# Optimization experiments

Hardware: AMD Instinct MI355X
Metric: run time of the kernel (lower is better)

The kernel has to match this reference:

```python
import jax, jax.numpy as jnp
import numpy as np

B, E, H, T = 32768, 64, 128, 12  # batch, embedding_dim, decoder_h_dim, pred_len


def setup_inputs() -> dict:
    key = jax.random.key(0)
    ks = jax.random.split(key, 13)
    f = lambda k, shape: jax.random.normal(k, shape, dtype=jnp.float32) * 0.05
    return {
        "last_pos": f(ks[0], (B, 2)),
        "last_pos_rel": f(ks[1], (B, 2)),
        "h0": f(ks[2], (1, B, H)),
        "c0": f(ks[3], (1, B, H)),
        "pred_ped_speed": jax.random.uniform(ks[4], (T, B, 1), dtype=jnp.float32),
        # spatial_embedding: Linear(3, E)
        "W_se": f(ks[5], (E, 3)),
        "b_se": f(ks[6], (E,)),
        # single-layer LSTM(E -> H), torch gate order [i, f, g, o]
        "W_ih": f(ks[7], (4 * H, E)),
        "W_hh": f(ks[8], (4 * H, H)),
        "b_ih": f(ks[9], (4 * H,)),
        "b_hh": f(ks[10], (4 * H,)),
        # hidden2pos: Linear(H, 2)
        "W_hp": f(ks[11], (2, H)),
        "b_hp": f(ks[12], (2,)),
    }


def reference(last_pos, last_pos_rel, h0, c0, pred_ped_speed,
              W_se, b_se, W_ih, W_hh, b_ih, b_hh, W_hp, b_hp):
    # train_or_test == 0 path: speed comes straight from pred_ped_speed
    Tlen = pred_ped_speed.shape[0]
    b_lstm = b_ih + b_hh
    # initial decoder input: embed concat([last_pos_rel, speed_0])  -> [B, E]
    x0 = jnp.concatenate([last_pos_rel, pred_ped_speed[0]], axis=1) @ W_se.T + b_se

    def step(carry, t):
        h, c, x, lp = carry  # h,c: [B,H]; x: [B,E]; lp: [B,2]
        gates = x @ W_ih.T + h @ W_hh.T + b_lstm           # [B, 4H]
        i, f_, g, o = jnp.split(gates, 4, axis=1)
        c = jax.nn.sigmoid(f_) * c + jax.nn.sigmoid(i) * jnp.tanh(g)
        h = jax.nn.sigmoid(o) * jnp.tanh(c)
        rel = h @ W_hp.T + b_hp                            # [B, 2]
        lp = rel + lp                                      # curr_pos -> last_pos
        # speed for next step; at final step torch keeps the previous speed
        spd = pred_ped_speed[jnp.minimum(t + 1, Tlen - 1)]
        x = jnp.concatenate([rel, spd], axis=1) @ W_se.T + b_se
        return (h, c, x, lp), rel

    (h, c, _, _), rels = jax.lax.scan(
        step, (h0[0], c0[0], x0, last_pos), jnp.arange(Tlen))
    # pred_traj_fake_rel: [T, B, 2]; final hidden state: [1, B, H]
    return rels, h[None]
```

## Files before the change

### kernel.cpp

```cpp
#include <hip/hip_runtime.h>

#define T_LEN 12
#define B_N   32768
#define H_N   128
#define E_N   64
#define K_N   192
#define LDK   200
#define BM    64

typedef __attribute__((ext_vector_type(8))) __bf16 bf16x8;
typedef __attribute__((ext_vector_type(8))) short  short8v;
typedef __attribute__((ext_vector_type(4))) float  f32x4;

__device__ __forceinline__ unsigned short f2bf(float f) {
  unsigned int u = __builtin_bit_cast(unsigned int, f);
  u += 0x7fffu + ((u >> 16) & 1u);
  return (unsigned short)(u >> 16);
}
__device__ __forceinline__ float bf2f(unsigned short h) {
  unsigned int u = ((unsigned int)h) << 16;
  return __builtin_bit_cast(float, u);
}
__device__ __forceinline__ float sigm(float x) {
  return __builtin_amdgcn_rcpf(1.f + __builtin_amdgcn_exp2f(-1.4426950408889634f * x));
}
__device__ __forceinline__ float tanh_(float x) {
  return 1.f - 2.f * __builtin_amdgcn_rcpf(__builtin_amdgcn_exp2f(2.8853900817779268f * x) + 1.f);
}

__global__ void prep_kernel(const float* __restrict__ Wih, const float* __restrict__ Whh,
                            const float* __restrict__ bih, const float* __restrict__ bhh,
                            unsigned short* __restrict__ Wc, float* __restrict__ bl) {
  int i = blockIdx.x * 256 + threadIdx.x;
  if (i < 4 * H_N) bl[i] = bih[i] + bhh[i];
  if (i < 4 * H_N * K_N) {
    int n = i / K_N, k = i - n * K_N;
    float v = (k < E_N) ? Wih[n * E_N + k] : Whh[n * H_N + (k - E_N)];
    Wc[i] = f2bf(v);
  }
}

__launch_bounds__(512, 2)
__global__ void decoder_kernel(const float* __restrict__ last_pos_rel,
                               const float* __restrict__ h0,
                               const float* __restrict__ c0,
                               const float* __restrict__ pps,
                               const float* __restrict__ W_se,
                               const float* __restrict__ b_se,
                               const float* __restrict__ W_hp,
                               const float* __restrict__ b_hp,
                               const unsigned short* __restrict__ Wc,
                               const float* __restrict__ bl,
                               float* __restrict__ out_rel,
                               float* __restrict__ out_h) {
  __shared__ unsigned short xh[BM * LDK];
  __shared__ float relbuf[BM * 2];
  __shared__ float whp[2 * H_N];

  const int tid  = threadIdx.x;
  const int w    = tid >> 6;
  const int l    = tid & 63;
  const int l15  = l & 15;
  const int lg   = l >> 4;
  const int brow = blockIdx.x * BM;
  const int nh   = w * 16 + l15;

  short8v bw[4][6];
#pragma unroll
  for (int g = 0; g < 4; ++g)
#pragma unroll
    for (int ks = 0; ks < 6; ++ks)
      bw[g][ks] = *(const short8v*)(Wc + (g * H_N + nh) * K_N + ks * 32 + lg * 8);

  float bgate[4];
#pragma unroll
  for (int g = 0; g < 4; ++g) bgate[g] = bl[g * H_N + nh];

  f32x4 cst[4];
#pragma unroll
  for (int mt = 0; mt < 4; ++mt)
#pragma unroll
    for (int r = 0; r < 4; ++r)
      cst[mt][r] = c0[(brow + mt * 16 + lg * 4 + r) * H_N + nh];

  if (tid < 2 * H_N) whp[tid] = W_hp[tid];
  for (int i = tid; i < BM * H_N; i += 512) {
    int row = i >> 7, n = i & (H_N - 1);
    xh[row * LDK + E_N + n] = f2bf(h0[(brow + row) * H_N + n]);
  }
  const int  xe   = tid & 63;
  const float wse0 = W_se[xe * 3 + 0], wse1 = W_se[xe * 3 + 1], wse2 = W_se[xe * 3 + 2];
  const float bse  = b_se[xe];
  const float bhp0 = b_hp[0], bhp1 = b_hp[1];

#pragma unroll
  for (int rr = 0; rr < 8; ++rr) {
    int row = (tid >> 6) * 8 + rr;
    float r0 = last_pos_rel[(brow + row) * 2 + 0];
    float r1 = last_pos_rel[(brow + row) * 2 + 1];
    float sp = pps[0 * B_N + brow + row];
    xh[row * LDK + xe] = f2bf(r0 * wse0 + r1 * wse1 + sp * wse2 + bse);
  }

#pragma unroll 1
  for (int t = 0; t < T_LEN; ++t) {
    __syncthreads();

    f32x4 acc[4][4];
#pragma unroll
    for (int g = 0; g < 4; ++g)
#pragma unroll
      for (int mt = 0; mt < 4; ++mt)
        acc[g][mt] = (f32x4){bgate[g], bgate[g], bgate[g], bgate[g]};

#pragma unroll
    for (int ks = 0; ks < 6; ++ks) {
      bf16x8 a[4];
#pragma unroll
      for (int mt = 0; mt < 4; ++mt)
        a[mt] = __builtin_bit_cast(bf16x8,
                 *(const short8v*)(xh + (mt * 16 + l15) * LDK + ks * 32 + lg * 8));
#pragma unroll
      for (int g = 0; g < 4; ++g)
#pragma unroll
        for (int mt = 0; mt < 4; ++mt)
          acc[g][mt] = __builtin_amdgcn_mfma_f32_16x16x32_bf16(
              a[mt], __builtin_bit_cast(bf16x8, bw[g][ks]), acc[g][mt], 0, 0, 0);
    }

    __syncthreads();

#pragma unroll
    for (int mt = 0; mt < 4; ++mt) {
#pragma unroll
      for (int r = 0; r < 4; ++r) {
        float gi = acc[0][mt][r], gf = acc[1][mt][r];
        float gg = acc[2][mt][r], go = acc[3][mt][r];
        float cn = sigm(gf) * cst[mt][r] + sigm(gi) * tanh_(gg);
        cst[mt][r] = cn;
        float h = sigm(go) * tanh_(cn);
        int row = mt * 16 + lg * 4 + r;
        xh[row * LDK + E_N + nh] = f2bf(h);
        if (t == T_LEN - 1) out_h[(brow + row) * H_N + nh] = h;
      }
    }

    __syncthreads();

    {
      int dot = tid >> 2, part = tid & 3;
      int row = dot >> 1, j = dot & 1;
      float s = 0.f;
      int n0 = part * 32;
#pragma unroll
      for (int n = 0; n < 32; ++n)
        s += bf2f(xh[row * LDK + E_N + n0 + n]) * whp[j * H_N + n0 + n];
      s += __shfl_xor(s, 1);
      s += __shfl_xor(s, 2);
      if (part == 0) relbuf[dot] = s + (j ? bhp1 : bhp0);
    }

    __syncthreads();

    if (tid < 2 * BM) out_rel[(size_t)t * B_N * 2 + brow * 2 + tid] = relbuf[tid];
    if (t < T_LEN - 1) {
#pragma unroll
      for (int rr = 0; rr < 8; ++rr) {
        int row = (tid >> 6) * 8 + rr;
        float r0 = relbuf[row * 2 + 0], r1 = relbuf[row * 2 + 1];
        float sp = pps[(t + 1) * B_N + brow + row];
        xh[row * LDK + xe] = f2bf(r0 * wse0 + r1 * wse1 + sp * wse2 + bse);
      }
    }
  }
}

extern "C" void kernel_launch(void* const* d_in, const int* in_sizes, int n_in,
                              void* d_out, int out_size, void* d_ws, size_t ws_size,
                              hipStream_t stream) {
  const float* last_pos_rel = (const float*)d_in[1];
  const float* h0   = (const float*)d_in[2];
  const float* c0   = (const float*)d_in[3];
  const float* pps  = (const float*)d_in[4];
  const float* W_se = (const float*)d_in[5];
  const float* b_se = (const float*)d_in[6];
  const float* W_ih = (const float*)d_in[7];
  const float* W_hh = (const float*)d_in[8];
  const float* b_ih = (const float*)d_in[9];
  const float* b_hh = (const float*)d_in[10];
  const float* W_hp = (const float*)d_in[11];
  const float* b_hp = (const float*)d_in[12];

  unsigned short* Wc = (unsigned short*)d_ws;
  float* bl = (float*)((char*)d_ws + (size_t)(4 * H_N) * K_N * sizeof(unsigned short));

  float* out_rel = (float*)d_out;
  float* out_h   = out_rel + (size_t)T_LEN * B_N * 2;

  hipLaunchKernelGGL(prep_kernel, dim3((4 * H_N * K_N + 255) / 256), dim3(256), 0, stream,
                     W_ih, W_hh, b_ih, b_hh, Wc, bl);
  hipLaunchKernelGGL(decoder_kernel, dim3(B_N / BM), dim3(512), 0, stream,
                     last_pos_rel, h0, c0, pps, W_se, b_se, W_hp, b_hp, Wc, bl,
                     out_rel, out_h);
}
```

Baseline: 263.5 us.

## Fold input embedding and hidden2pos into recurrent weights, halve block rows

Folds the spatial embedding and hidden2pos projections algebraically into a single 512x128 recurrent matrix, so each step multiplies only h (K=128 instead of 192), plus a per-row speed term and a first-step correction. Half of the fused weights now live in swizzled LDS and half in registers. The rel output is computed with an extra small MFMA one step later. The block tile drops to 32 rows with launch bounds raised to 4 blocks per CU, and two per-step barriers plus the scalar dot-product pass are removed. The folded weights are rounded to bf16 after combining, which shifts numerical error slightly.

```diff
diff --git a/kernel.cpp b/kernel.cpp
--- a/kernel.cpp
+++ b/kernel.cpp
@@ -4,9 +4,7 @@
 #define B_N   32768
 #define H_N   128
 #define E_N   64
-#define K_N   192
-#define LDK   200
-#define BM    64
+#define BM    32
 
 typedef __attribute__((ext_vector_type(8))) __bf16 bf16x8;
 typedef __attribute__((ext_vector_type(8))) short  short8v;
@@ -17,10 +15,6 @@
   u += 0x7fffu + ((u >> 16) & 1u);
   return (unsigned short)(u >> 16);
 }
-__device__ __forceinline__ float bf2f(unsigned short h) {
-  unsigned int u = ((unsigned int)h) << 16;
-  return __builtin_bit_cast(float, u);
-}
 __device__ __forceinline__ float sigm(float x) {
   return __builtin_amdgcn_rcpf(1.f + __builtin_amdgcn_exp2f(-1.4426950408889634f * x));
 }
@@ -30,32 +24,54 @@
 
 __global__ void prep_kernel(const float* __restrict__ Wih, const float* __restrict__ Whh,
                             const float* __restrict__ bih, const float* __restrict__ bhh,
-                            unsigned short* __restrict__ Wc, float* __restrict__ bl) {
+                            const float* __restrict__ Wse, const float* __restrict__ bse,
+                            const float* __restrict__ Whp, const float* __restrict__ bhp,
+                            unsigned short* __restrict__ Wf, float* __restrict__ u,
+                            float* __restrict__ w0, float* __restrict__ G) {
   int i = blockIdx.x * 256 + threadIdx.x;
-  if (i < 4 * H_N) bl[i] = bih[i] + bhh[i];
-  if (i < 4 * H_N * K_N) {
-    int n = i / K_N, k = i - n * K_N;
-    float v = (k < E_N) ? Wih[n * E_N + k] : Whh[n * H_N + (k - E_N)];
-    Wc[i] = f2bf(v);
-  }
-}
-
-__launch_bounds__(512, 2)
-__global__ void decoder_kernel(const float* __restrict__ last_pos_rel,
+  if (i < 512 * 128) {
+    int n = i >> 7, k = i & 127;
+    float s = Whh[n * 128 + k];
+    float wh0 = Whp[k], wh1 = Whp[128 + k];
+    for (int e = 0; e < 64; ++e)
+      s += Wih[n * 64 + e] * (Wse[e * 3 + 0] * wh0 + Wse[e * 3 + 1] * wh1);
+    Wf[i] = f2bf(s);
+  } else if (i < 512 * 128 + 2048) {
+    int j = i - 512 * 128;
+    int n = j >> 2, which = j & 3;
+    float s = 0.f;
+    if (which < 2) {
+      for (int e = 0; e < 64; ++e) s += Wih[n * 64 + e] * Wse[e * 3 + which];
+      G[n * 2 + which] = s;
+    } else if (which == 2) {
+      for (int e = 0; e < 64; ++e) s += Wih[n * 64 + e] * Wse[e * 3 + 2];
+      u[n] = s;
+    } else {
+      for (int e = 0; e < 64; ++e)
+        s += Wih[n * 64 + e] * (bse[e] + Wse[e * 3 + 0] * bhp[0] + Wse[e * 3 + 1] * bhp[1]);
+      w0[n] = bih[n] + bhh[n] + s;
+    }
+  }
+}
+
+__launch_bounds__(512, 4)
+__global__ void decoder_kernel(const float* __restrict__ lpr,
                                const float* __restrict__ h0,
                                const float* __restrict__ c0,
                                const float* __restrict__ pps,
-                               const float* __restrict__ W_se,
-                               const float* __restrict__ b_se,
-                               const float* __restrict__ W_hp,
-                               const float* __restrict__ b_hp,
-                               const unsigned short* __restrict__ Wc,
-                               const float* __restrict__ bl,
+                               const float* __restrict__ Whp,
+                               const float* __restrict__ bhp,
+                               const unsigned short* __restrict__ Wf,
+                               const float* __restrict__ u,
+                               const float* __restrict__ w0,
+                               const float* __restrict__ G,
                                float* __restrict__ out_rel,
                                float* __restrict__ out_h) {
-  __shared__ unsigned short xh[BM * LDK];
-  __shared__ float relbuf[BM * 2];
-  __shared__ float whp[2 * H_N];
+  __shared__ unsigned short WfL[256 * 128];
+  __shared__ unsigned short hS[BM * 128];
+  __shared__ unsigned short whpB[4 * 64 * 8];
+  __shared__ float spdbuf[BM];
+  __shared__ float dbuf[BM * 2];
 
   const int tid  = threadIdx.x;
   const int w    = tid >> 6;
@@ -64,113 +80,147 @@
   const int lg   = l >> 4;
   const int brow = blockIdx.x * BM;
   const int nh   = w * 16 + l15;
-
-  short8v bw[4][6];
-#pragma unroll
-  for (int g = 0; g < 4; ++g)
-#pragma unroll
-    for (int ks = 0; ks < 6; ++ks)
-      bw[g][ks] = *(const short8v*)(Wc + (g * H_N + nh) * K_N + ks * 32 + lg * 8);
-
-  float bgate[4];
-#pragma unroll
-  for (int g = 0; g < 4; ++g) bgate[g] = bl[g * H_N + nh];
-
-  f32x4 cst[4];
-#pragma unroll
-  for (int mt = 0; mt < 4; ++mt)
+  const int swz  = (l15 & 7) << 4;
+  char* hB  = (char*)hS;
+  char* wB  = (char*)WfL;
+  char* pB  = (char*)whpB;
+
+  for (int i = tid; i < 256 * 16; i += 512) {
+    int row = i >> 4, k16 = i & 15;
+    short8v v = *(const short8v*)(Wf + (256 + row) * 128 + k16 * 8);
+    int byte = (row * 256 + k16 * 16) ^ ((row & 7) << 4);
+    *(short8v*)(wB + byte) = v;
+  }
+  short8v bw[2][4];
+#pragma unroll
+  for (int g = 0; g < 2; ++g)
+#pragma unroll
+    for (int ks = 0; ks < 4; ++ks)
+      bw[g][ks] = *(const short8v*)(Wf + (g * 128 + nh) * 128 + ks * 32 + lg * 8);
+
+  float ur[4], w0r[4];
+#pragma unroll
+  for (int g = 0; g < 4; ++g) { ur[g] = u[g * 128 + nh]; w0r[g] = w0[g * 128 + nh]; }
+
+  f32x4 cst[2];
+#pragma unroll
+  for (int mt = 0; mt < 2; ++mt)
 #pragma unroll
     for (int r = 0; r < 4; ++r)
       cst[mt][r] = c0[(brow + mt * 16 + lg * 4 + r) * H_N + nh];
 
-  if (tid < 2 * H_N) whp[tid] = W_hp[tid];
-  for (int i = tid; i < BM * H_N; i += 512) {
-    int row = i >> 7, n = i & (H_N - 1);
-    xh[row * LDK + E_N + n] = f2bf(h0[(brow + row) * H_N + n]);
-  }
-  const int  xe   = tid & 63;
-  const float wse0 = W_se[xe * 3 + 0], wse1 = W_se[xe * 3 + 1], wse2 = W_se[xe * 3 + 2];
-  const float bse  = b_se[xe];
-  const float bhp0 = b_hp[0], bhp1 = b_hp[1];
-
-#pragma unroll
-  for (int rr = 0; rr < 8; ++rr) {
-    int row = (tid >> 6) * 8 + rr;
-    float r0 = last_pos_rel[(brow + row) * 2 + 0];
-    float r1 = last_pos_rel[(brow + row) * 2 + 1];
-    float sp = pps[0 * B_N + brow + row];
-    xh[row * LDK + xe] = f2bf(r0 * wse0 + r1 * wse1 + sp * wse2 + bse);
-  }
+  {
+    int row = tid >> 4, k0 = (tid & 15) * 8;
+    const float* src = h0 + (brow + row) * H_N + k0;
+    unsigned short tmp[8];
+#pragma unroll
+    for (int j = 0; j < 8; ++j) tmp[j] = f2bf(src[j]);
+    int byte = (row * 256 + k0 * 2) ^ ((row & 7) << 4);
+    *(short8v*)(hB + byte) = *(short8v*)tmp;
+  }
+  if (tid < 256) {
+    int ks = tid >> 6, ll = tid & 63, c = ll & 15, kg = ll >> 4;
+    unsigned short tmp[8];
+#pragma unroll
+    for (int j = 0; j < 8; ++j)
+      tmp[j] = (c < 2) ? f2bf(Whp[c * 128 + ks * 32 + kg * 8 + j]) : (unsigned short)0;
+    *(short8v*)(pB + (ks * 64 + ll) * 16) = *(short8v*)tmp;
+  }
+  {
+    int dot = tid >> 3, part = tid & 7;
+    int row = dot >> 1, j = dot & 1;
+    float s = 0.f;
+    const float* hrow = h0 + (brow + row) * H_N + part * 16;
+    const float* wrow = Whp + j * 128 + part * 16;
+#pragma unroll
+    for (int k = 0; k < 16; ++k) s += hrow[k] * wrow[k];
+    s += __shfl_xor(s, 1); s += __shfl_xor(s, 2); s += __shfl_xor(s, 4);
+    if (part == 0) dbuf[dot] = lpr[(brow + row) * 2 + j] - bhp[j] - s;
+  }
+  const float bhpr = (l15 < 2) ? bhp[l15] : 0.f;
 
 #pragma unroll 1
   for (int t = 0; t < T_LEN; ++t) {
     __syncthreads();
 
-    f32x4 acc[4][4];
+    if (tid < BM) spdbuf[tid] = pps[t * B_N + brow + tid];
+
+    f32x4 acc[4][2];
 #pragma unroll
     for (int g = 0; g < 4; ++g)
 #pragma unroll
-      for (int mt = 0; mt < 4; ++mt)
-        acc[g][mt] = (f32x4){bgate[g], bgate[g], bgate[g], bgate[g]};
-
-#pragma unroll
-    for (int ks = 0; ks < 6; ++ks) {
-      bf16x8 a[4];
-#pragma unroll
-      for (int mt = 0; mt < 4; ++mt)
-        a[mt] = __builtin_bit_cast(bf16x8,
-                 *(const short8v*)(xh + (mt * 16 + l15) * LDK + ks * 32 + lg * 8));
-#pragma unroll
-      for (int g = 0; g < 4; ++g)
-#pragma unroll
-        for (int mt = 0; mt < 4; ++mt)
-          acc[g][mt] = __builtin_amdgcn_mfma_f32_16x16x32_bf16(
-              a[mt], __builtin_bit_cast(bf16x8, bw[g][ks]), acc[g][mt], 0, 0, 0);
+      for (int mt = 0; mt < 2; ++mt) acc[g][mt] = (f32x4){0.f, 0.f, 0.f, 0.f};
+    f32x4 relC = (f32x4){0.f, 0.f, 0.f, 0.f};
+
+#pragma unroll
+    for (int ks = 0; ks < 4; ++ks) {
+      int kb = ks * 64 + lg * 16;
+      bf16x8 a0 = __builtin_bit_cast(bf16x8, *(short8v*)(hB + ((l15 * 256 + kb) ^ swz)));
+      bf16x8 a1 = __builtin_bit_cast(bf16x8, *(short8v*)(hB + (((16 + l15) * 256 + kb) ^ swz)));
+      bf16x8 b2 = __builtin_bit_cast(bf16x8, *(short8v*)(wB + ((nh * 256 + kb) ^ swz)));
+      bf16x8 b3 = __builtin_bit_cast(bf16x8, *(short8v*)(wB + 32768 + ((nh * 256 + kb) ^ swz)));
+      acc[0][0] = __builtin_amdgcn_mfma_f32_16x16x32_bf16(a0, __builtin_bit_cast(bf16x8, bw[0][ks]), acc[0][0], 0, 0, 0);
+      acc[0][1] = __builtin_amdgcn_mfma_f32_16x16x32_bf16(a1, __builtin_bit_cast(bf16x8, bw[0][ks]), acc[0][1], 0, 0, 0);
+      acc[1][0] = __builtin_amdgcn_mfma_f32_16x16x32_bf16(a0, __builtin_bit_cast(bf16x8, bw[1][ks]), acc[1][0], 0, 0, 0);
+      acc[1][1] = __builtin_amdgcn_mfma_f32_16x16x32_bf16(a1, __builtin_bit_cast(bf16x8, bw[1][ks]), acc[1][1], 0, 0, 0);
+      acc[2][0] = __builtin_amdgcn_mfma_f32_16x16x32_bf16(a0, b2, acc[2][0], 0, 0, 0);
+      acc[2][1] = __builtin_amdgcn_mfma_f32_16x16x32_bf16(a1, b2, acc[2][1], 0, 0, 0);
+      acc[3][0] = __builtin_amdgcn_mfma_f32_16x16x32_bf16(a0, b3, acc[3][0], 0, 0, 0);
+      acc[3][1] = __builtin_amdgcn_mfma_f32_16x16x32_bf16(a1, b3, acc[3][1], 0, 0, 0);
+      if (w < 2 && t > 0) {
+        bf16x8 wb = __builtin_bit_cast(bf16x8, *(short8v*)(pB + ks * 1024 + l * 16));
+        relC = __builtin_amdgcn_mfma_f32_16x16x32_bf16(w == 0 ? a0 : a1, wb, relC, 0, 0, 0);
+      }
+    }
+    if (w < 2 && t > 0 && l15 < 2) {
+#pragma unroll
+      for (int r = 0; r < 4; ++r)
+        out_rel[(size_t)(t - 1) * B_N * 2 + (brow + w * 16 + lg * 4 + r) * 2 + l15] = relC[r] + bhpr;
     }
 
     __syncthreads();
 
 #pragma unroll
-    for (int mt = 0; mt < 4; ++mt) {
+    for (int mt = 0; mt < 2; ++mt) {
 #pragma unroll
       for (int r = 0; r < 4; ++r) {
-        float gi = acc[0][mt][r], gf = acc[1][mt][r];
-        float gg = acc[2][mt][r], go = acc[3][mt][r];
+        int row = mt * 16 + lg * 4 + r;
+        float spd = spdbuf[row];
+        float gi = acc[0][mt][r] + w0r[0] + spd * ur[0];
+        float gf = acc[1][mt][r] + w0r[1] + spd * ur[1];
+        float gg = acc[2][mt][r] + w0r[2] + spd * ur[2];
+        float go = acc[3][mt][r] + w0r[3] + spd * ur[3];
+        if (t == 0) {
+          float d0 = dbuf[row * 2 + 0], d1 = dbuf[row * 2 + 1];
+          gi += d0 * G[(0 * 128 + nh) * 2 + 0] + d1 * G[(0 * 128 + nh) * 2 + 1];
+          gf += d0 * G[(1 * 128 + nh) * 2 + 0] + d1 * G[(1 * 128 + nh) * 2 + 1];
+          gg += d0 * G[(2 * 128 + nh) * 2 + 0] + d1 * G[(2 * 128 + nh) * 2 + 1];
+          go += d0 * G[(3 * 128 + nh) * 2 + 0] + d1 * G[(3 * 128 + nh) * 2 + 1];
+        }
         float cn = sigm(gf) * cst[mt][r] + sigm(gi) * tanh_(gg);
         cst[mt][r] = cn;
         float h = sigm(go) * tanh_(cn);
-        int row = mt * 16 + lg * 4 + r;
-        xh[row * LDK + E_N + nh] = f2bf(h);
+        hS[((row * 256 + nh * 2) ^ ((row & 7) << 4)) >> 1] = f2bf(h);
         if (t == T_LEN - 1) out_h[(brow + row) * H_N + nh] = h;
       }
     }
-
-    __syncthreads();
-
-    {
-      int dot = tid >> 2, part = tid & 3;
-      int row = dot >> 1, j = dot & 1;
-      float s = 0.f;
-      int n0 = part * 32;
-#pragma unroll
-      for (int n = 0; n < 32; ++n)
-        s += bf2f(xh[row * LDK + E_N + n0 + n]) * whp[j * H_N + n0 + n];
-      s += __shfl_xor(s, 1);
-      s += __shfl_xor(s, 2);
-      if (part == 0) relbuf[dot] = s + (j ? bhp1 : bhp0);
-    }
-
-    __syncthreads();
-
-    if (tid < 2 * BM) out_rel[(size_t)t * B_N * 2 + brow * 2 + tid] = relbuf[tid];
-    if (t < T_LEN - 1) {
-#pragma unroll
-      for (int rr = 0; rr < 8; ++rr) {
-        int row = (tid >> 6) * 8 + rr;
-        float r0 = relbuf[row * 2 + 0], r1 = relbuf[row * 2 + 1];
-        float sp = pps[(t + 1) * B_N + brow + row];
-        xh[row * LDK + xe] = f2bf(r0 * wse0 + r1 * wse1 + sp * wse2 + bse);
-      }
+  }
+
+  __syncthreads();
+  if (w < 2) {
+    f32x4 relC = (f32x4){0.f, 0.f, 0.f, 0.f};
+#pragma unroll
+    for (int ks = 0; ks < 4; ++ks) {
+      int kb = ks * 64 + lg * 16;
+      bf16x8 a = __builtin_bit_cast(bf16x8,
+          *(short8v*)(hB + (((w * 16 + l15) * 256 + kb) ^ swz)));
+      bf16x8 wb = __builtin_bit_cast(bf16x8, *(short8v*)(pB + ks * 1024 + l * 16));
+      relC = __builtin_amdgcn_mfma_f32_16x16x32_bf16(a, wb, relC, 0, 0, 0);
+    }
+    if (l15 < 2) {
+#pragma unroll
+      for (int r = 0; r < 4; ++r)
+        out_rel[(size_t)(T_LEN - 1) * B_N * 2 + (brow + w * 16 + lg * 4 + r) * 2 + l15] = relC[r] + bhpr;
     }
   }
 }
@@ -178,7 +228,7 @@
 extern "C" void kernel_launch(void* const* d_in, const int* in_sizes, int n_in,
                               void* d_out, int out_size, void* d_ws, size_t ws_size,
                               hipStream_t stream) {
-  const float* last_pos_rel = (const float*)d_in[1];
+  const float* lpr  = (const float*)d_in[1];
   const float* h0   = (const float*)d_in[2];
   const float* c0   = (const float*)d_in[3];
   const float* pps  = (const float*)d_in[4];
@@ -191,15 +241,16 @@
   const float* W_hp = (const float*)d_in[11];
   const float* b_hp = (const float*)d_in[12];
 
-  unsigned short* Wc = (unsigned short*)d_ws;
-  float* bl = (float*)((char*)d_ws + (size_t)(4 * H_N) * K_N * sizeof(unsigned short));
+  unsigned short* Wf = (unsigned short*)d_ws;
+  float* u  = (float*)((char*)d_ws + 131072);
+  float* w0 = (float*)((char*)d_ws + 133120);
+  float* G  = (float*)((char*)d_ws + 135168);
 
   float* out_rel = (float*)d_out;
   float* out_h   = out_rel + (size_t)T_LEN * B_N * 2;
 
-  hipLaunchKernelGGL(prep_kernel, dim3((4 * H_N * K_N + 255) / 256), dim3(256), 0, stream,
-                     W_ih, W_hh, b_ih, b_hh, Wc, bl);
+  hipLaunchKernelGGL(prep_kernel, dim3((512 * 128 + 2048 + 255) / 256), dim3(256), 0, stream,
+                     W_ih, W_hh, b_ih, b_hh, W_se, b_se, W_hp, b_hp, Wf, u, w0, G);
   hipLaunchKernelGGL(decoder_kernel, dim3(B_N / BM), dim3(512), 0, stream,
-                     last_pos_rel, h0, c0, pps, W_se, b_se, W_hp, b_hp, Wc, bl,
-                     out_rel, out_h);
-}
+                     lpr, h0, c0, pps, W_hp, b_hp, Wf, u, w0, G, out_rel, out_h);
+}
```

Measured after the change: 261.8 us. About the same (-0.7%).
